# Performance work log

Measured on AMD Instinct MI355X. Metric: run time of the kernel, lower is better.

Reference implementation:

```python
import jax, jax.numpy as jnp
import numpy as np

B, S, D = 4, 2048, 256
H = 8
HD = D // H
DFF = 512
EPS_CUTOFF = 1e-15
LN_EPS = 1e-5


def _layer_norm(x, gamma, beta):
    mu = jnp.mean(x, axis=-1, keepdims=True)
    var = jnp.mean(jnp.square(x - mu), axis=-1, keepdims=True)
    return (x - mu) * jax.lax.rsqrt(var + LN_EPS) * gamma + beta


def setup_inputs() -> dict:
    key = jax.random.key(0)
    ks = jax.random.split(key, 12)
    s = 1.0 / np.sqrt(D)
    inp = {
        "tokens": jax.random.normal(ks[0], (B, S, D), dtype=jnp.float32),
        "cutoff_factors": jax.random.uniform(ks[1], (B, S, S), dtype=jnp.float32),
        "Wqkv": jax.random.uniform(ks[2], (3 * D, D), jnp.float32, -s, s),
        "bqkv": jnp.zeros((3 * D,), jnp.float32),
        "Wo": jax.random.uniform(ks[3], (D, D), jnp.float32, -s, s),
        "bo": jnp.zeros((D,), jnp.float32),
        "ln1_g": jnp.ones((D,), jnp.float32),
        "ln1_b": jnp.zeros((D,), jnp.float32),
        "ln2_g": jnp.ones((D,), jnp.float32),
        "ln2_b": jnp.zeros((D,), jnp.float32),
        "W1": jax.random.uniform(ks[4], (DFF, D), jnp.float32, -s, s),
        "b1": jax.random.uniform(ks[5], (DFF,), jnp.float32, -s, s),
        "W2": jax.random.uniform(ks[6], (D, DFF), jnp.float32, -1.0 / np.sqrt(DFF), 1.0 / np.sqrt(DFF)),
        "b2": jax.random.uniform(ks[7], (D,), jnp.float32, -1.0 / np.sqrt(DFF), 1.0 / np.sqrt(DFF)),
        "use_manual_attention": 1,
    }
    return inp


def reference(tokens, cutoff_factors, Wqkv, bqkv, Wo, bo, ln1_g, ln1_b, ln2_g, ln2_b, W1, b1, W2, b2, use_manual_attention):
    # --- attention block ---
    qkv = tokens @ Wqkv.T + bqkv                      # [B,S,3D]
    qkv = qkv.reshape(B, S, 3, H, HD).transpose(2, 0, 3, 1, 4)  # [3,B,H,S,HD]
    q, k, v = qkv[0], qkv[1], qkv[2]
    attn_mask = jnp.log(jnp.clip(cutoff_factors, EPS_CUTOFF))[:, None, :, :]  # [B,1,S,S]
    scores = jnp.einsum("bhqd,bhkd->bhqk", q, k) / np.sqrt(HD) + attn_mask
    probs = jax.nn.softmax(scores, axis=-1)
    attn = jnp.einsum("bhqk,bhkd->bhqd", probs, v)    # [B,H,S,HD]
    attn = attn.transpose(0, 2, 1, 3).reshape(B, S, D)
    attn = attn @ Wo.T + bo
    # --- PostLN residual + norm ---
    x = _layer_norm(tokens + attn, ln1_g, ln1_b)
    # --- MLP (SiLU) ---
    h = jax.nn.silu(x @ W1.T + b1)
    mlp_out = h @ W2.T + b2
    return _layer_norm(x + mlp_out, ln2_g, ln2_b)
```

## Files before the change

kernel.cpp:

```cpp
#include <hip/hip_runtime.h>
#include <hip/hip_bf16.h>
#include <math.h>

#define B_ 4
#define S_ 2048
#define D_ 256
#define H_ 8
#define HD_ 32
#define DFF_ 512

typedef __attribute__((ext_vector_type(8))) short bf16x8;
typedef __attribute__((ext_vector_type(4))) float f32x4;

__device__ inline short f2bf(float f) {
  union { float f; unsigned u; } x; x.f = f;
  unsigned r = (x.u + 0x7FFFu + ((x.u >> 16) & 1u)) >> 16;
  return (short)r;
}
__device__ inline float bf2f(short s) {
  union { unsigned u; float f; } x; x.u = ((unsigned)(unsigned short)s) << 16;
  return x.f;
}
__device__ inline unsigned cvt_pk_bf16(float a, float b) {
  unsigned r;
  asm("v_cvt_pk_bf16_f32 %0, %1, %2" : "=v"(r) : "v"(a), "v"(b));
  return r;
}
__device__ inline float exp2v(float x) {
  float r;
  asm("v_exp_f32 %0, %1" : "=v"(r) : "v"(x));
  return r;
}

__global__ __launch_bounds__(256) void cvt_all(const float* __restrict__ tok, const float* __restrict__ wq,
                                               const float* __restrict__ wo, const float* __restrict__ w1,
                                               const float* __restrict__ w2,
                                               short* __restrict__ dtok, short* __restrict__ dwq,
                                               short* __restrict__ dwo, short* __restrict__ dw1,
                                               short* __restrict__ dw2) {
  int blk = blockIdx.x;
  const float* src; short* dst; int base;
  if (blk < 2048)      { src = tok; dst = dtok; base = blk; }
  else if (blk < 2240) { src = wq;  dst = dwq;  base = blk - 2048; }
  else if (blk < 2304) { src = wo;  dst = dwo;  base = blk - 2240; }
  else if (blk < 2432) { src = w1;  dst = dw1;  base = blk - 2304; }
  else                 { src = w2;  dst = dw2;  base = blk - 2432; }
  int i = (base * 256 + threadIdx.x) * 4;
  float4 v = *(const float4*)(src + i);
  short4 s; s.x = f2bf(v.x); s.y = f2bf(v.y); s.z = f2bf(v.z); s.w = f2bf(v.w);
  *(short4*)(dst + i) = s;
}

template<int MODE>
__global__ __launch_bounds__(256) void gemm_bf(const short* __restrict__ A,
                                               const short* __restrict__ W,
                                               const float* __restrict__ bias,
                                               float* __restrict__ Cf,
                                               short* __restrict__ Cb,
                                               int M, int N, int K) {
  constexpr int BM = 128, BN = 64;
  __shared__ short As[BM][72];
  __shared__ short Bs[BN][72];
  const int tid = threadIdx.x;
  const int wid = tid >> 6, lane = tid & 63;
  const int g = lane >> 4, lc = lane & 15;
  const int wr = wid >> 1, wc = wid & 1;
  const int rowBase = blockIdx.y * BM;
  const int colBase = blockIdx.x * BN;

  f32x4 acc[4][2];
#pragma unroll
  for (int m = 0; m < 4; ++m)
#pragma unroll
    for (int n = 0; n < 2; ++n) { acc[m][n][0]=0.f; acc[m][n][1]=0.f; acc[m][n][2]=0.f; acc[m][n][3]=0.f; }

  for (int k0 = 0; k0 < K; k0 += 64) {
    __syncthreads();
#pragma unroll
    for (int i = 0; i < 4; ++i) {
      int task = tid + 256 * i;
      int r = task >> 3, c = (task & 7) * 8;
      *(bf16x8*)&As[r][c] = *(const bf16x8*)(A + (size_t)(rowBase + r) * K + k0 + c);
    }
#pragma unroll
    for (int i = 0; i < 2; ++i) {
      int task = tid + 256 * i;
      int r = task >> 3, c = (task & 7) * 8;
      *(bf16x8*)&Bs[r][c] = *(const bf16x8*)(W + (size_t)(colBase + r) * K + k0 + c);
    }
    __syncthreads();
#pragma unroll
    for (int ks = 0; ks < 2; ++ks) {
      bf16x8 af[4], bfr[2];
#pragma unroll
      for (int m = 0; m < 4; ++m) af[m] = *(const bf16x8*)&As[wr*64 + m*16 + lc][ks*32 + g*8];
#pragma unroll
      for (int n = 0; n < 2; ++n) bfr[n] = *(const bf16x8*)&Bs[wc*32 + n*16 + lc][ks*32 + g*8];
#pragma unroll
      for (int m = 0; m < 4; ++m)
#pragma unroll
        for (int n = 0; n < 2; ++n)
          acc[m][n] = __builtin_amdgcn_mfma_f32_16x16x32_bf16(af[m], bfr[n], acc[m][n], 0, 0, 0);
    }
  }

#pragma unroll
  for (int m = 0; m < 4; ++m)
#pragma unroll
    for (int n = 0; n < 2; ++n) {
      int col = colBase + wc*32 + n*16 + lc;
      float bv = bias[col];
      int row0 = rowBase + wr*64 + m*16 + g*4;
      float vj[4];
#pragma unroll
      for (int j = 0; j < 4; ++j) vj[j] = acc[m][n][j] + bv;
      if (MODE == 1) {
#pragma unroll
        for (int j = 0; j < 4; ++j) {
          float v = vj[j];
          v = v / (1.f + __expf(-v));
          Cb[(size_t)(row0 + j) * N + col] = f2bf(v);
        }
      } else {
        int part = col >> 8;
        int h = (col >> 5) & 7;
        int hd = col & 31;
        int b = row0 >> 11, s0 = row0 & 2047;
        if (part == 2) {
          short4 s4;
          s4.x = f2bf(vj[0]); s4.y = f2bf(vj[1]); s4.z = f2bf(vj[2]); s4.w = f2bf(vj[3]);
          *(short4*)(Cb + 2 * 2097152 + (((size_t)b * 8 + h) * 32 + hd) * 2048 + s0) = s4;
        } else {
          float sc = (part == 0) ? 0.25506807f : 1.f;
#pragma unroll
          for (int j = 0; j < 4; ++j)
            Cb[(size_t)part * 2097152 + (((size_t)b * 8 + h) * 2048 + s0 + j) * 32 + hd] = f2bf(vj[j] * sc);
        }
      }
    }
}

__global__ __launch_bounds__(256) void gemm_bf64(const short* __restrict__ A,
                                                 const short* __restrict__ W,
                                                 const float* __restrict__ bias,
                                                 float* __restrict__ Cf,
                                                 int M, int N, int K) {
  __shared__ short As[64][72];
  __shared__ short Bs[64][72];
  const int tid = threadIdx.x;
  const int wid = tid >> 6, lane = tid & 63;
  const int g = lane >> 4, lc = lane & 15;
  const int wr = wid >> 1, wc = wid & 1;
  const int rowBase = blockIdx.y * 64;
  const int colBase = blockIdx.x * 64;

  f32x4 acc[2][2];
#pragma unroll
  for (int m = 0; m < 2; ++m)
#pragma unroll
    for (int n = 0; n < 2; ++n) { acc[m][n][0]=0.f; acc[m][n][1]=0.f; acc[m][n][2]=0.f; acc[m][n][3]=0.f; }

  for (int k0 = 0; k0 < K; k0 += 64) {
    __syncthreads();
#pragma unroll
    for (int i = 0; i < 2; ++i) {
      int task = tid + 256 * i;
      int r = task >> 3, c = (task & 7) * 8;
      *(bf16x8*)&As[r][c] = *(const bf16x8*)(A + (size_t)(rowBase + r) * K + k0 + c);
      *(bf16x8*)&Bs[r][c] = *(const bf16x8*)(W + (size_t)(colBase + r) * K + k0 + c);
    }
    __syncthreads();
#pragma unroll
    for (int ks = 0; ks < 2; ++ks) {
      bf16x8 af[2], bfr[2];
#pragma unroll
      for (int m = 0; m < 2; ++m) af[m] = *(const bf16x8*)&As[wr*32 + m*16 + lc][ks*32 + g*8];
#pragma unroll
      for (int n = 0; n < 2; ++n) bfr[n] = *(const bf16x8*)&Bs[wc*32 + n*16 + lc][ks*32 + g*8];
#pragma unroll
      for (int m = 0; m < 2; ++m)
#pragma unroll
        for (int n = 0; n < 2; ++n)
          acc[m][n] = __builtin_amdgcn_mfma_f32_16x16x32_bf16(af[m], bfr[n], acc[m][n], 0, 0, 0);
    }
  }

#pragma unroll
  for (int m = 0; m < 2; ++m)
#pragma unroll
    for (int n = 0; n < 2; ++n) {
      int col = colBase + wc*32 + n*16 + lc;
      float bv = bias[col];
      int row0 = rowBase + wr*32 + m*16 + g*4;
#pragma unroll
      for (int j = 0; j < 4; ++j)
        Cf[(size_t)(row0 + j) * N + col] = acc[m][n][j] + bv;
    }
}

__global__ __launch_bounds__(256) void knorm_max(const short* __restrict__ kbf, unsigned* __restrict__ kmax) {
  const int bh = blockIdx.x >> 3;
  const int r = (blockIdx.x & 7) * 256 + threadIdx.x;
  const short* kp = kbf + ((size_t)bh * S_ + r) * HD_;
  float ss = 0.f;
#pragma unroll
  for (int c = 0; c < 4; ++c) {
    bf16x8 v = *(const bf16x8*)(kp + c * 8);
#pragma unroll
    for (int j = 0; j < 8; ++j) { float f = bf2f(v[j]); ss = fmaf(f, f, ss); }
  }
#pragma unroll
  for (int o = 1; o < 64; o <<= 1) ss = fmaxf(ss, __shfl_xor(ss, o, 64));
  __shared__ float red[4];
  if ((threadIdx.x & 63) == 0) red[threadIdx.x >> 6] = ss;
  __syncthreads();
  if (threadIdx.x == 0) {
    float mx = fmaxf(fmaxf(red[0], red[1]), fmaxf(red[2], red[3]));
    atomicMax(kmax + bh, __float_as_uint(mx));
  }
}

__global__ __launch_bounds__(256) void q_mfix(const short* __restrict__ qbf,
                                              const unsigned* __restrict__ kmax,
                                              float* __restrict__ mfix) {
  const int bh = blockIdx.x >> 3;
  const int r = (blockIdx.x & 7) * 256 + threadIdx.x;
  const short* qp = qbf + ((size_t)bh * S_ + r) * HD_;
  float ss = 0.f;
#pragma unroll
  for (int c = 0; c < 4; ++c) {
    bf16x8 v = *(const bf16x8*)(qp + c * 8);
#pragma unroll
    for (int j = 0; j < 8; ++j) { float f = bf2f(v[j]); ss = fmaf(f, f, ss); }
  }
  mfix[(size_t)bh * S_ + r] = sqrtf(ss * __uint_as_float(kmax[bh]));
}

__global__ __launch_bounds__(256, 4) void attn_mfma(const short* __restrict__ qbf,
                                                    const short* __restrict__ kbf,
                                                    const short* __restrict__ vtbf,
                                                    const float* __restrict__ cutoff,
                                                    const float* __restrict__ mfix,
                                                    short* __restrict__ outbf) {
  constexpr int KB = 64;
  const int qt = blockIdx.x & 31;
  const int h  = (blockIdx.x >> 5) & 7;
  const int b  = blockIdx.x >> 8;
  const int tid = threadIdx.x;
  const int wid = tid >> 6, lane = tid & 63;
  const int g = lane >> 4, lc = lane & 15;

  __shared__ __align__(16) short Ks[2][KB][56];
  __shared__ __align__(16) short Vt[2][HD_][72];
  __shared__ __align__(16) short Pq[4][16][72];

  const int bh = b * H_ + h;
  const int qrow = qt * 64 + wid * 16 + lc;
  const short* qg = qbf + (size_t)bh * S_ * HD_;
  const short* kg = kbf + (size_t)bh * S_ * HD_;
  const short* vg = vtbf + (size_t)bh * HD_ * S_;

  bf16x8 qf = *(const bf16x8*)(qg + (size_t)qrow * HD_ + g * 8);
  const float m = mfix[(size_t)bh * S_ + qrow];

  f32x4 oacc[2];
#pragma unroll
  for (int d = 0; d < 2; ++d) { oacc[d][0]=0.f; oacc[d][1]=0.f; oacc[d][2]=0.f; oacc[d][3]=0.f; }
  float sml = 0.f;

  const float* cb = cutoff + ((size_t)(b * S_) + qrow) * (size_t)S_;

  const int kr = tid >> 2, kc = (tid & 3) * 8;
  const int vr = tid >> 3, vc = (tid & 7) * 8;
  const short* kptr = kg + (size_t)kr * HD_ + kc;
  const short* vptr = vg + (size_t)vr * S_ + vc;

  bf16x8 kreg = *(const bf16x8*)kptr;
  bf16x8 vreg = *(const bf16x8*)vptr;
  *(bf16x8*)&Ks[0][kr][kc] = kreg;
  *(bf16x8*)&Vt[0][vr][vc] = vreg;
  float4 cv[4];
#pragma unroll
  for (int t = 0; t < 4; ++t) cv[t] = *(const float4*)(cb + t * 16 + g * 4);
  __syncthreads();

  int cur = 0;
#pragma unroll 2
  for (int kt = 0; kt < S_; kt += KB) {
    const bool notlast = (kt + KB < S_);
    if (notlast) {
      kreg = *(const bf16x8*)(kptr + (size_t)(kt + KB) * HD_);
      vreg = *(const bf16x8*)(vptr + (kt + KB));
    }

    bf16x8 kf[4];
#pragma unroll
    for (int t = 0; t < 4; ++t) kf[t] = *(const bf16x8*)&Ks[cur][t*16 + lc][g*8];
    f32x4 st[4];
#pragma unroll
    for (int t = 0; t < 4; ++t) {
      f32x4 z = {0.f, 0.f, 0.f, 0.f};
      st[t] = __builtin_amdgcn_mfma_f32_16x16x32_bf16(kf[t], qf, z, 0, 0, 0);
    }

    float4 cvn[4];
    if (notlast) {
#pragma unroll
      for (int t = 0; t < 4; ++t) cvn[t] = *(const float4*)(cb + kt + KB + t * 16 + g * 4);
    }

#pragma unroll
    for (int t = 0; t < 4; ++t) {
      float p0 = cv[t].x * exp2v(st[t][0] - m);
      float p1 = cv[t].y * exp2v(st[t][1] - m);
      float p2 = cv[t].z * exp2v(st[t][2] - m);
      float p3 = cv[t].w * exp2v(st[t][3] - m);
      sml += (p0 + p1) + (p2 + p3);
      uint2 pk;
      pk.x = cvt_pk_bf16(p0, p1);
      pk.y = cvt_pk_bf16(p2, p3);
      *(uint2*)&Pq[wid][lc][t*16 + g*4] = pk;
    }

    asm volatile("s_waitcnt lgkmcnt(0)" ::: "memory");
    __builtin_amdgcn_sched_barrier(0);

#pragma unroll
    for (int kh = 0; kh < 2; ++kh) {
      bf16x8 pb = *(const bf16x8*)&Pq[wid][lc][kh*32 + g*8];
#pragma unroll
      for (int dh = 0; dh < 2; ++dh) {
        bf16x8 va = *(const bf16x8*)&Vt[cur][dh*16 + lc][kh*32 + g*8];
        oacc[dh] = __builtin_amdgcn_mfma_f32_16x16x32_bf16(va, pb, oacc[dh], 0, 0, 0);
      }
    }

    if (notlast) {
      __syncthreads();
      *(bf16x8*)&Ks[cur ^ 1][kr][kc] = kreg;
      *(bf16x8*)&Vt[cur ^ 1][vr][vc] = vreg;
      __syncthreads();
      cur ^= 1;
#pragma unroll
      for (int t = 0; t < 4; ++t) cv[t] = cvn[t];
    }
  }

  float s = sml;
  s += __shfl_xor(s, 16, 64);
  s += __shfl_xor(s, 32, 64);
  float inv = 1.f / s;
#pragma unroll
  for (int dh = 0; dh < 2; ++dh) {
    uint2 pk;
    pk.x = cvt_pk_bf16(oacc[dh][0] * inv, oacc[dh][1] * inv);
    pk.y = cvt_pk_bf16(oacc[dh][2] * inv, oacc[dh][3] * inv);
    *(uint2*)(outbf + ((size_t)(b * S_) + qrow) * D_ + h * HD_ + dh * 16 + g * 4) = pk;
  }
}

template<int WBF>
__global__ __launch_bounds__(256) void residual_ln(const float* __restrict__ xa,
                                                   const float* __restrict__ xb,
                                                   const float* __restrict__ g,
                                                   const float* __restrict__ bt,
                                                   float* __restrict__ out,
                                                   short* __restrict__ outbf) {
  const int row  = blockIdx.x * 4 + (threadIdx.x >> 6);
  const int lane = threadIdx.x & 63;
  float4 va = *(const float4*)(xa + (size_t)row * D_ + lane * 4);
  float4 vb = *(const float4*)(xb + (size_t)row * D_ + lane * 4);
  float v[4] = {va.x + vb.x, va.y + vb.y, va.z + vb.z, va.w + vb.w};
  float s = v[0] + v[1] + v[2] + v[3];
#pragma unroll
  for (int o = 32; o > 0; o >>= 1) s += __shfl_xor(s, o, 64);
  float mu = s * (1.f / D_);
  float var = 0.f;
#pragma unroll
  for (int i = 0; i < 4; ++i) { v[i] -= mu; var += v[i] * v[i]; }
#pragma unroll
  for (int o = 32; o > 0; o >>= 1) var += __shfl_xor(var, o, 64);
  float rs = rsqrtf(var * (1.f / D_) + 1e-5f);
  float4 g4 = *(const float4*)(g + lane * 4);
  float4 b4 = *(const float4*)(bt + lane * 4);
  float4 o4 = {v[0] * rs * g4.x + b4.x, v[1] * rs * g4.y + b4.y,
               v[2] * rs * g4.z + b4.z, v[3] * rs * g4.w + b4.w};
  *(float4*)(out + (size_t)row * D_ + lane * 4) = o4;
  if (WBF) {
    short4 s4; s4.x = f2bf(o4.x); s4.y = f2bf(o4.y); s4.z = f2bf(o4.z); s4.w = f2bf(o4.w);
    *(short4*)(outbf + (size_t)row * D_ + lane * 4) = s4;
  }
}

extern "C" void kernel_launch(void* const* d_in, const int* in_sizes, int n_in,
                              void* d_out, int out_size, void* d_ws, size_t ws_size,
                              hipStream_t stream) {
  const float* tokens = (const float*)d_in[0];
  const float* cutoff = (const float*)d_in[1];
  const float* Wqkv   = (const float*)d_in[2];
  const float* bqkv   = (const float*)d_in[3];
  const float* Wo     = (const float*)d_in[4];
  const float* bo     = (const float*)d_in[5];
  const float* ln1g   = (const float*)d_in[6];
  const float* ln1b   = (const float*)d_in[7];
  const float* ln2g   = (const float*)d_in[8];
  const float* ln2b   = (const float*)d_in[9];
  const float* W1     = (const float*)d_in[10];
  const float* b1     = (const float*)d_in[11];
  const float* W2     = (const float*)d_in[12];
  const float* b2     = (const float*)d_in[13];
  float* out = (float*)d_out;

  char* w = (char*)d_ws;
  const size_t MB = 1 << 20;
  short* qbf    = (short*)w;
  short* kbf    = qbf + 2097152;
  short* vtbf   = qbf + 2 * 2097152;
  short* tokbf  = (short*)(w + 12 * MB);
  short* wq_bf  = (short*)(w + 16 * MB);
  short* wo_bf  = wq_bf + 196608;
  short* w1_bf  = wo_bf + 65536;
  short* w2_bf  = w1_bf + 131072;
  short* attnbf = tokbf;
  float* projOut = (float*)(w + 18 * MB);
  float* xbuf    = (float*)(w + 26 * MB);
  float* mfix    = (float*)(w + 34 * MB);
  unsigned* kmax = (unsigned*)(w + 34 * MB + 262144);
  short* xbbf    = qbf;
  short* hbbf    = kbf;
  float* mlpOut  = projOut;

  const int M = B_ * S_;

  cvt_all<<<dim3(2560), 256, 0, stream>>>(tokens, Wqkv, Wo, W1, W2, tokbf, wq_bf, wo_bf, w1_bf, w2_bf);
  hipMemsetAsync(kmax, 0, 128, stream);

  gemm_bf<2><<<dim3(12, 64), 256, 0, stream>>>(tokbf, wq_bf, bqkv, nullptr, qbf, M, 3 * D_, D_);
  knorm_max<<<dim3(256), 256, 0, stream>>>(kbf, kmax);
  q_mfix<<<dim3(256), 256, 0, stream>>>(qbf, kmax, mfix);
  attn_mfma<<<dim3(1024), 256, 0, stream>>>(qbf, kbf, vtbf, cutoff, mfix, attnbf);
  gemm_bf64<<<dim3(4, 128), 256, 0, stream>>>(attnbf, wo_bf, bo, projOut, M, D_, D_);
  residual_ln<1><<<dim3(M / 4), 256, 0, stream>>>(tokens, projOut, ln1g, ln1b, xbuf, xbbf);
  gemm_bf<1><<<dim3(8, 64), 256, 0, stream>>>(xbbf, w1_bf, b1, nullptr, hbbf, M, DFF_, D_);
  gemm_bf64<<<dim3(4, 128), 256, 0, stream>>>(hbbf, w2_bf, b2, mlpOut, M, D_, DFF_);
  residual_ln<0><<<dim3(M / 4), 256, 0, stream>>>(xbuf, mlpOut, ln2g, ln2b, out, nullptr);
}
```

Baseline: 142.2 us.

## Fuse key-norm max into QKV GEMM and compute query bound inside attention

The per-head max squared key norm is now computed in the QKV GEMM epilogue with shuffles and an atomicMax. The query-norm softmax bound is computed directly in the attention kernel from the loaded query fragment, which removes two separate kernel launches and their extra reads of Q and K. The K shared-memory tile is shrunk to 32 columns with an XOR swizzle to avoid bank conflicts, and the exponent argument is clamped to 8. The norm is now taken from fp32 values before bf16 rounding, which could change the bound slightly, and the clamp guards against overflow from that.

```diff
diff --git a/kernel.cpp b/kernel.cpp
--- a/kernel.cpp
+++ b/kernel.cpp
@@ -57,6 +57,7 @@
                                                const float* __restrict__ bias,
                                                float* __restrict__ Cf,
                                                short* __restrict__ Cb,
+                                               unsigned* __restrict__ kmaxp,
                                                int M, int N, int K) {
   constexpr int BM = 128, BN = 64;
   __shared__ short As[BM][72];
@@ -104,8 +105,11 @@
     }
   }
 
-#pragma unroll
-  for (int m = 0; m < 4; ++m)
+  const int part = (colBase + wc * 32) >> 8;
+  float rmax = 0.f;
+#pragma unroll
+  for (int m = 0; m < 4; ++m) {
+    float nsum[4] = {0.f, 0.f, 0.f, 0.f};
 #pragma unroll
     for (int n = 0; n < 2; ++n) {
       int col = colBase + wc*32 + n*16 + lc;
@@ -122,7 +126,6 @@
           Cb[(size_t)(row0 + j) * N + col] = f2bf(v);
         }
       } else {
-        int part = col >> 8;
         int h = (col >> 5) & 7;
         int hd = col & 31;
         int b = row0 >> 11, s0 = row0 & 2047;
@@ -135,9 +138,32 @@
 #pragma unroll
           for (int j = 0; j < 4; ++j)
             Cb[(size_t)part * 2097152 + (((size_t)b * 8 + h) * 2048 + s0 + j) * 32 + hd] = f2bf(vj[j] * sc);
+          if (part == 1) {
+#pragma unroll
+            for (int j = 0; j < 4; ++j) nsum[j] = fmaf(vj[j], vj[j], nsum[j]);
+          }
         }
       }
     }
+    if (MODE == 2 && part == 1) {
+#pragma unroll
+      for (int j = 0; j < 4; ++j) {
+        float t = nsum[j];
+        t += __shfl_xor(t, 1, 64); t += __shfl_xor(t, 2, 64);
+        t += __shfl_xor(t, 4, 64); t += __shfl_xor(t, 8, 64);
+        rmax = fmaxf(rmax, t);
+      }
+    }
+  }
+  if (MODE == 2 && part == 1) {
+    rmax = fmaxf(rmax, __shfl_xor(rmax, 16, 64));
+    rmax = fmaxf(rmax, __shfl_xor(rmax, 32, 64));
+    if (lane == 0) {
+      int h = ((colBase + wc * 32) >> 5) & 7;
+      int b = rowBase >> 11;
+      atomicMax(kmaxp + b * 8 + h, __float_as_uint(rmax));
+    }
+  }
 }
 
 __global__ __launch_bounds__(256) void gemm_bf64(const short* __restrict__ A,
@@ -198,49 +224,11 @@
     }
 }
 
-__global__ __launch_bounds__(256) void knorm_max(const short* __restrict__ kbf, unsigned* __restrict__ kmax) {
-  const int bh = blockIdx.x >> 3;
-  const int r = (blockIdx.x & 7) * 256 + threadIdx.x;
-  const short* kp = kbf + ((size_t)bh * S_ + r) * HD_;
-  float ss = 0.f;
-#pragma unroll
-  for (int c = 0; c < 4; ++c) {
-    bf16x8 v = *(const bf16x8*)(kp + c * 8);
-#pragma unroll
-    for (int j = 0; j < 8; ++j) { float f = bf2f(v[j]); ss = fmaf(f, f, ss); }
-  }
-#pragma unroll
-  for (int o = 1; o < 64; o <<= 1) ss = fmaxf(ss, __shfl_xor(ss, o, 64));
-  __shared__ float red[4];
-  if ((threadIdx.x & 63) == 0) red[threadIdx.x >> 6] = ss;
-  __syncthreads();
-  if (threadIdx.x == 0) {
-    float mx = fmaxf(fmaxf(red[0], red[1]), fmaxf(red[2], red[3]));
-    atomicMax(kmax + bh, __float_as_uint(mx));
-  }
-}
-
-__global__ __launch_bounds__(256) void q_mfix(const short* __restrict__ qbf,
-                                              const unsigned* __restrict__ kmax,
-                                              float* __restrict__ mfix) {
-  const int bh = blockIdx.x >> 3;
-  const int r = (blockIdx.x & 7) * 256 + threadIdx.x;
-  const short* qp = qbf + ((size_t)bh * S_ + r) * HD_;
-  float ss = 0.f;
-#pragma unroll
-  for (int c = 0; c < 4; ++c) {
-    bf16x8 v = *(const bf16x8*)(qp + c * 8);
-#pragma unroll
-    for (int j = 0; j < 8; ++j) { float f = bf2f(v[j]); ss = fmaf(f, f, ss); }
-  }
-  mfix[(size_t)bh * S_ + r] = sqrtf(ss * __uint_as_float(kmax[bh]));
-}
-
 __global__ __launch_bounds__(256, 4) void attn_mfma(const short* __restrict__ qbf,
                                                     const short* __restrict__ kbf,
                                                     const short* __restrict__ vtbf,
                                                     const float* __restrict__ cutoff,
-                                                    const float* __restrict__ mfix,
+                                                    const unsigned* __restrict__ kmaxp,
                                                     short* __restrict__ outbf) {
   constexpr int KB = 64;
   const int qt = blockIdx.x & 31;
@@ -250,7 +238,7 @@
   const int wid = tid >> 6, lane = tid & 63;
   const int g = lane >> 4, lc = lane & 15;
 
-  __shared__ __align__(16) short Ks[2][KB][56];
+  __shared__ __align__(16) short Ks[2][KB][32];
   __shared__ __align__(16) short Vt[2][HD_][72];
   __shared__ __align__(16) short Pq[4][16][72];
 
@@ -261,7 +249,13 @@
   const short* vg = vtbf + (size_t)bh * HD_ * S_;
 
   bf16x8 qf = *(const bf16x8*)(qg + (size_t)qrow * HD_ + g * 8);
-  const float m = mfix[(size_t)bh * S_ + qrow];
+
+  float ssq = 0.f;
+#pragma unroll
+  for (int i = 0; i < 8; ++i) { float f = bf2f(qf[i]); ssq = fmaf(f, f, ssq); }
+  ssq += __shfl_xor(ssq, 16, 64);
+  ssq += __shfl_xor(ssq, 32, 64);
+  const float m = sqrtf(ssq * __uint_as_float(kmaxp[bh]));
 
   f32x4 oacc[2];
 #pragma unroll
@@ -270,14 +264,16 @@
 
   const float* cb = cutoff + ((size_t)(b * S_) + qrow) * (size_t)S_;
 
-  const int kr = tid >> 2, kc = (tid & 3) * 8;
-  const int vr = tid >> 3, vc = (tid & 7) * 8;
-  const short* kptr = kg + (size_t)kr * HD_ + kc;
+  const int kr = tid >> 2;
+  const int kslot = ((tid & 3) ^ ((kr >> 1) & 3)) * 8;
+  const short* kptr = kg + (size_t)kr * HD_ + (tid & 3) * 8;
+  const int vr = tid >> 3;
+  const int vc = (tid & 7) * 8;
   const short* vptr = vg + (size_t)vr * S_ + vc;
 
   bf16x8 kreg = *(const bf16x8*)kptr;
   bf16x8 vreg = *(const bf16x8*)vptr;
-  *(bf16x8*)&Ks[0][kr][kc] = kreg;
+  *(bf16x8*)&Ks[0][kr][kslot] = kreg;
   *(bf16x8*)&Vt[0][vr][vc] = vreg;
   float4 cv[4];
 #pragma unroll
@@ -295,7 +291,8 @@
 
     bf16x8 kf[4];
 #pragma unroll
-    for (int t = 0; t < 4; ++t) kf[t] = *(const bf16x8*)&Ks[cur][t*16 + lc][g*8];
+    for (int t = 0; t < 4; ++t)
+      kf[t] = *(const bf16x8*)&Ks[cur][t*16 + lc][(g ^ ((lc >> 1) & 3)) * 8];
     f32x4 st[4];
 #pragma unroll
     for (int t = 0; t < 4; ++t) {
@@ -311,10 +308,10 @@
 
 #pragma unroll
     for (int t = 0; t < 4; ++t) {
-      float p0 = cv[t].x * exp2v(st[t][0] - m);
-      float p1 = cv[t].y * exp2v(st[t][1] - m);
-      float p2 = cv[t].z * exp2v(st[t][2] - m);
-      float p3 = cv[t].w * exp2v(st[t][3] - m);
+      float p0 = cv[t].x * exp2v(fminf(st[t][0] - m, 8.f));
+      float p1 = cv[t].y * exp2v(fminf(st[t][1] - m, 8.f));
+      float p2 = cv[t].z * exp2v(fminf(st[t][2] - m, 8.f));
+      float p3 = cv[t].w * exp2v(fminf(st[t][3] - m, 8.f));
       sml += (p0 + p1) + (p2 + p3);
       uint2 pk;
       pk.x = cvt_pk_bf16(p0, p1);
@@ -337,7 +334,7 @@
 
     if (notlast) {
       __syncthreads();
-      *(bf16x8*)&Ks[cur ^ 1][kr][kc] = kreg;
+      *(bf16x8*)&Ks[cur ^ 1][kr][kslot] = kreg;
       *(bf16x8*)&Vt[cur ^ 1][vr][vc] = vreg;
       __syncthreads();
       cur ^= 1;
@@ -424,24 +421,21 @@
   short* attnbf = tokbf;
   float* projOut = (float*)(w + 18 * MB);
   float* xbuf    = (float*)(w + 26 * MB);
-  float* mfix    = (float*)(w + 34 * MB);
-  unsigned* kmax = (unsigned*)(w + 34 * MB + 262144);
+  unsigned* kmax = (unsigned*)(w + 34 * MB);
   short* xbbf    = qbf;
   short* hbbf    = kbf;
   float* mlpOut  = projOut;
 
   const int M = B_ * S_;
 
+  hipMemsetAsync(kmax, 0, 128, stream);
   cvt_all<<<dim3(2560), 256, 0, stream>>>(tokens, Wqkv, Wo, W1, W2, tokbf, wq_bf, wo_bf, w1_bf, w2_bf);
-  hipMemsetAsync(kmax, 0, 128, stream);
-
-  gemm_bf<2><<<dim3(12, 64), 256, 0, stream>>>(tokbf, wq_bf, bqkv, nullptr, qbf, M, 3 * D_, D_);
-  knorm_max<<<dim3(256), 256, 0, stream>>>(kbf, kmax);
-  q_mfix<<<dim3(256), 256, 0, stream>>>(qbf, kmax, mfix);
-  attn_mfma<<<dim3(1024), 256, 0, stream>>>(qbf, kbf, vtbf, cutoff, mfix, attnbf);
+
+  gemm_bf<2><<<dim3(12, 64), 256, 0, stream>>>(tokbf, wq_bf, bqkv, nullptr, qbf, kmax, M, 3 * D_, D_);
+  attn_mfma<<<dim3(1024), 256, 0, stream>>>(qbf, kbf, vtbf, cutoff, kmax, attnbf);
   gemm_bf64<<<dim3(4, 128), 256, 0, stream>>>(attnbf, wo_bf, bo, projOut, M, D_, D_);
   residual_ln<1><<<dim3(M / 4), 256, 0, stream>>>(tokens, projOut, ln1g, ln1b, xbuf, xbbf);
-  gemm_bf<1><<<dim3(8, 64), 256, 0, stream>>>(xbbf, w1_bf, b1, nullptr, hbbf, M, DFF_, D_);
+  gemm_bf<1><<<dim3(8, 64), 256, 0, stream>>>(xbbf, w1_bf, b1, nullptr, hbbf, nullptr, M, DFF_, D_);
   gemm_bf64<<<dim3(4, 128), 256, 0, stream>>>(hbbf, w2_bf, b2, mlpOut, M, D_, DFF_);
   residual_ln<0><<<dim3(M / 4), 256, 0, stream>>>(xbuf, mlpOut, ln2g, ln2b, out, nullptr);
 }
```

After: 145.2 us. +2.1%, slower.
